# Optimization experiments

Measured on AMD Instinct MI355X. Metric: run time of the kernel, lower is better.

## Reference

```python
import jax, jax.numpy as jnp
import numpy as np

N0, N1, N2 = 100000, 20000, 4000   # nodes per hierarchy level
F, H, C = 128, 128, 10             # num_features, hidden_dim, num_classes
E0, E1, E2 = 1600000, 320000, 64000  # intra-level edges (avg degree 16)
EPS = 1e-5                          # BatchNorm eps


def setup_inputs() -> dict:
    key = jax.random.key(0)
    ks = jax.random.split(key, 16)
    s = 0.05
    return {
        "x": jax.random.normal(ks[0], (N0, F), jnp.float32),
        "ei0": jax.random.randint(ks[1], (2, E0), 0, N0),
        "ei1": jax.random.randint(ks[2], (2, E1), 0, N1),
        "ei2": jax.random.randint(ks[3], (2, E2), 0, N2),
        "parent1": jax.random.randint(ks[4], (N0,), 0, N1),
        "parent2": jax.random.randint(ks[5], (N1,), 0, N2),
        "W0": jax.random.normal(ks[6], (F, H), jnp.float32) * s,
        "b0": jnp.zeros((H,), jnp.float32),
        "W1": jax.random.normal(ks[7], (H, H), jnp.float32) * s,
        "b1": jnp.zeros((H,), jnp.float32),
        "W2": jax.random.normal(ks[8], (H, H), jnp.float32) * s,
        "b2": jnp.zeros((H,), jnp.float32),
        "W3": jax.random.normal(ks[9], (2 * H, H), jnp.float32) * s,
        "b3": jnp.zeros((H,), jnp.float32),
        "W4": jax.random.normal(ks[10], (2 * H, C), jnp.float32) * s,
        "b4": jnp.zeros((C,), jnp.float32),
        "pW": jax.random.normal(ks[11], (4, H, H), jnp.float32) * s,
        "pb": jnp.zeros((4, H), jnp.float32),
        "pgamma": jnp.ones((4, H), jnp.float32),
        "pbeta": jnp.zeros((4, H), jnp.float32),
        "pmean": jax.random.normal(ks[12], (4, H), jnp.float32) * 0.1,
        "pvar": jax.random.uniform(ks[13], (4, H), jnp.float32, 0.5, 1.5),
    }


def _gcn(x, ei, W, b):
    # GCNConv: add self loops, symmetric D^-1/2 (A+I) D^-1/2 normalization.
    n = x.shape[0]
    loops = jnp.arange(n)
    row = jnp.concatenate([ei[0], loops])  # source nodes
    col = jnp.concatenate([ei[1], loops])  # target nodes
    deg = jax.ops.segment_sum(jnp.ones(row.shape, x.dtype), col, num_segments=n)
    dis = deg ** -0.5  # deg >= 1 because of self loops
    norm = dis[row] * dis[col]
    xw = x @ W
    out = jax.ops.segment_sum(norm[:, None] * xw[row], col, num_segments=n)
    return out + b


def _pool_nn(y, W, b, g, beta, mean, var):
    # SEPooling nn: Linear -> ReLU -> BatchNorm1d (eval mode, running stats)
    y = jax.nn.relu(y @ W + b)
    return (y - mean) * (g / jnp.sqrt(var + EPS)) + beta


def reference(x, ei0, ei1, ei2, parent1, parent2,
              W0, b0, W1, b1, W2, b2, W3, b3, W4, b4,
              pW, pb, pgamma, pbeta, pmean, pvar):
    relu = jax.nn.relu
    # down path (dropout is identity in eval mode)
    h0 = relu(_gcn(x, ei0, W0, b0))  # [N0,H]; stored skip xs[0]
    p = jax.ops.segment_sum(h0, parent1, num_segments=N1)  # scatter-add children -> parents
    x1 = relu(_pool_nn(p, pW[0], pb[0], pgamma[0], pbeta[0], pmean[0], pvar[0]))
    h1 = relu(_gcn(x1, ei1, W1, b1))  # [N1,H]; stored skip xs[1]
    p = jax.ops.segment_sum(h1, parent2, num_segments=N2)
    x2 = relu(_pool_nn(p, pW[1], pb[1], pgamma[1], pbeta[1], pmean[1], pvar[1]))
    # up path: conv, unpool (gather parent feature per child), concat skip
    h = relu(_gcn(x2, ei2, W2, b2))  # [N2,H]
    xu = relu(_pool_nn(h[parent2], pW[2], pb[2], pgamma[2], pbeta[2], pmean[2], pvar[2]))  # [N1,H]
    xc = jnp.concatenate([xu, h1], axis=1)  # [N1,2H]
    h = relu(_gcn(xc, ei1, W3, b3))  # [N1,H]
    xu = relu(_pool_nn(h[parent1], pW[3], pb[3], pgamma[3], pbeta[3], pmean[3], pvar[3]))  # [N0,H]
    xc = jnp.concatenate([xu, h0], axis=1)  # [N0,2H]
    out = _gcn(xc, ei0, W4, b4)  # [N0,C]
    return jax.nn.log_softmax(out, axis=-1)
```

## Files before the change

### kernel.cpp

```cpp
#include <hip/hip_runtime.h>
#include <math.h>

#define N0 100000
#define N1 20000
#define N2 4000
#define HDIM 128
#define E0C 1600000
#define E1C 320000
#define E2C 64000
#define EPSBN 1e-5f

typedef unsigned int u32;
typedef float f32x4 __attribute__((ext_vector_type(4)));
typedef short bf16x8 __attribute__((ext_vector_type(8)));

union FragU { uint4 u; bf16x8 h; };
__device__ __forceinline__ bf16x8 asbf(uint4 v) { FragU x; x.u = v; return x.h; }

__device__ __forceinline__ float bl(u32 p) { return __uint_as_float(p << 16); }
__device__ __forceinline__ float bh(u32 p) { return __uint_as_float(p & 0xFFFF0000u); }
__device__ __forceinline__ u32 pack2(float a, float b) {
    u32 ua = __float_as_uint(a), ub = __float_as_uint(b);
    ua = (ua + 0x7FFFu + ((ua >> 16) & 1u)) >> 16;
    ub = (ub + 0x7FFFu + ((ub >> 16) & 1u)) >> 16;
    return ua | (ub << 16);
}

#define OFF0 0
#define OFF1 (N0)
#define OFF2 (N0 + N1)
#define OFF3 (N0 + N1 + N2)
#define OFF4 (N0 + N1 + N2 + N1)
#define OFFT (N0 + N1 + N2 + N1 + N2)

#define S0 (E0C)
#define S1 (E0C + E1C)
#define S2 (E0C + E1C + E2C)
#define S3 (E0C + E1C + E2C + N0)
#define S4 (E0C + E1C + E2C + N0 + N1)

#define NBUCK ((OFFT + 1023) / 1024)
#define ITEMS_PER_BLK 2048
#define NBA ((S4 + ITEMS_PER_BLK - 1) / ITEMS_PER_BLK)
#define BH_N (NBUCK * NBA)
#define NBLK2 ((BH_N + 1023) / 1024)


__device__ __forceinline__ void item_full(int g,
    const int* __restrict__ ei0r, const int* __restrict__ ei0c,
    const int* __restrict__ ei1r, const int* __restrict__ ei1c,
    const int* __restrict__ ei2r, const int* __restrict__ ei2c,
    const int* __restrict__ p1, const int* __restrict__ p2,
    int& concat, int& payload)
{
    if (g < S0)      { concat = ei0c[g];             payload = ei0r[g]; }
    else if (g < S1) { int i = g - S0; concat = OFF1 + ei1c[i]; payload = ei1r[i]; }
    else if (g < S2) { int i = g - S1; concat = OFF2 + ei2c[i]; payload = ei2r[i]; }
    else if (g < S3) { int i = g - S2; concat = OFF3 + p1[i];   payload = i; }
    else             { int i = g - S3; concat = OFF4 + p2[i];   payload = i; }
}

__device__ __forceinline__ int item_concat(int g,
    const int* __restrict__ ei0c, const int* __restrict__ ei1c, const int* __restrict__ ei2c,
    const int* __restrict__ p1, const int* __restrict__ p2)
{
    if (g < S0)      return ei0c[g];
    else if (g < S1) return OFF1 + ei1c[g - S0];
    else if (g < S2) return OFF2 + ei2c[g - S1];
    else if (g < S3) return OFF3 + p1[g - S2];
    else             return OFF4 + p2[g - S3];
}

__global__ __launch_bounds__(256) void binhist_kernel(
    const int* __restrict__ ei0c, const int* __restrict__ ei1c, const int* __restrict__ ei2c,
    const int* __restrict__ p1, const int* __restrict__ p2,
    int* __restrict__ blockHist)
{
    __shared__ int hist[NBUCK];
    int tid = threadIdx.x, blk = blockIdx.x;
    for (int i = tid; i < NBUCK; i += 256) hist[i] = 0;
    __syncthreads();
    int base = blk * ITEMS_PER_BLK;
    #pragma unroll
    for (int k = 0; k < ITEMS_PER_BLK / 256; k++) {
        int g = base + k * 256 + tid;
        if (g < S4) {
            int c = item_concat(g, ei0c, ei1c, ei2c, p1, p2);
            atomicAdd(&hist[c >> 10], 1);
        }
    }
    __syncthreads();
    for (int b = tid; b < NBUCK; b += 256) blockHist[b * NBA + blk] = hist[b];
}

__global__ __launch_bounds__(256) void scan_k1(const int* __restrict__ c, int* __restrict__ bsum, int n) {
    int t = threadIdx.x;
    int base = blockIdx.x * 1024 + t * 4;
    int s = 0;
    #pragma unroll
    for (int j = 0; j < 4; j++) {
        int idx = base + j;
        if (idx < n) s += c[idx];
    }
    #pragma unroll
    for (int o = 32; o > 0; o >>= 1) s += __shfl_down(s, o, 64);
    __shared__ int ws[4];
    if ((t & 63) == 0) ws[t >> 6] = s;
    __syncthreads();
    if (t == 0) bsum[blockIdx.x] = ws[0] + ws[1] + ws[2] + ws[3];
}

__global__ __launch_bounds__(256) void scan_k2(int* __restrict__ bsum, int* __restrict__ totalOut, int nb) {
    int t = threadIdx.x;
    int v = (t < nb) ? bsum[t] : 0;
    __shared__ int ts[256];
    ts[t] = v;
    __syncthreads();
    for (int o = 1; o < 256; o <<= 1) {
        int u = (t >= o) ? ts[t - o] : 0;
        __syncthreads();
        ts[t] += u;
        __syncthreads();
    }
    if (t < nb) bsum[t] = ts[t] - v;
    if (t == nb - 1) *totalOut = ts[t];
}

__global__ __launch_bounds__(256) void scan_k3(const int* __restrict__ c, const int* __restrict__ bsum,
                                               const int* __restrict__ total,
                                               int* __restrict__ S, int n) {
    int t = threadIdx.x;
    int base = blockIdx.x * 1024 + t * 4;
    int v[4];
    #pragma unroll
    for (int j = 0; j < 4; j++) v[j] = (base + j < n) ? c[base + j] : 0;
    int tsum = v[0] + v[1] + v[2] + v[3];
    __shared__ int ts[256];
    ts[t] = tsum;
    __syncthreads();
    for (int o = 1; o < 256; o <<= 1) {
        int u = (t >= o) ? ts[t - o] : 0;
        __syncthreads();
        ts[t] += u;
        __syncthreads();
    }
    int run = bsum[blockIdx.x] + ts[t] - tsum;
    #pragma unroll
    for (int j = 0; j < 4; j++) {
        if (base + j < n) { S[base + j] = run; run += v[j]; }
    }
    if (blockIdx.x == 0 && t == 0) S[n] = *total;
}

__global__ __launch_bounds__(256) void binfill_kernel(
    const int* __restrict__ ei0r, const int* __restrict__ ei0c,
    const int* __restrict__ ei1r, const int* __restrict__ ei1c,
    const int* __restrict__ ei2r, const int* __restrict__ ei2c,
    const int* __restrict__ p1, const int* __restrict__ p2,
    const int* __restrict__ OfsAbs, u32* __restrict__ binPair)
{
    __shared__ int cur[NBUCK];
    int tid = threadIdx.x, blk = blockIdx.x;
    for (int i = tid; i < NBUCK; i += 256) cur[i] = OfsAbs[i * NBA + blk];
    __syncthreads();
    int base = blk * ITEMS_PER_BLK;
    #pragma unroll
    for (int k = 0; k < ITEMS_PER_BLK / 256; k++) {
        int g = base + k * 256 + tid;
        if (g < S4) {
            int c, p;
            item_full(g, ei0r, ei0c, ei1r, ei1c, ei2r, ei2c, p1, p2, c, p);
            int pos = atomicAdd(&cur[c >> 10], 1);
            binPair[pos] = ((u32)(c & 1023) << 17) | (u32)p;
        }
    }
}

__global__ __launch_bounds__(1024) void bucket_build_kernel(
    const u32* __restrict__ binPair, const int* __restrict__ OfsAbs,
    int* __restrict__ rpAll, int* __restrict__ srcU,
    float* __restrict__ dis0, float* __restrict__ dis1, float* __restrict__ dis2)
{
    __shared__ int cnt_l[1024];
    __shared__ int rp_l[1024];
    __shared__ int ts2[1024];
    int b = blockIdx.x, tid = threadIdx.x;
    int start = OfsAbs[b * NBA];
    int end = (b + 1 < NBUCK) ? OfsAbs[(b + 1) * NBA] : S4;
    int d0 = b << 10;
    int nd = OFFT - d0; if (nd > 1024) nd = 1024;

    cnt_l[tid] = 0;
    __syncthreads();
    for (int i = start + tid; i < end; i += 1024) {
        u32 e = binPair[i];
        atomicAdd(&cnt_l[e >> 17], 1);
    }
    __syncthreads();
    int v = cnt_l[tid];
    ts2[tid] = v;
    __syncthreads();
    for (int o = 1; o < 1024; o <<= 1) {
        int u = (tid >= o) ? ts2[tid - o] : 0;
        __syncthreads();
        ts2[tid] += u;
        __syncthreads();
    }
    rp_l[tid] = ts2[tid] - v;
    __syncthreads();
    if (tid < nd) {
        int g = d0 + tid;
        rpAll[g] = start + rp_l[tid];
        float dv = rsqrtf((float)(v + 1));
        if (g < OFF1) dis0[g] = dv;
        else if (g < OFF2) dis1[g - OFF1] = dv;
        else if (g < OFF3) dis2[g - OFF2] = dv;
    }
    if (b == NBUCK - 1 && tid == 0) rpAll[OFFT] = S4;
    __syncthreads();
    for (int i = start + tid; i < end; i += 1024) {
        u32 e = binPair[i];
        int pos = start + atomicAdd(&rp_l[e >> 17], 1);
        srcU[pos] = (int)(e & 0x1FFFFu);
    }
}

__global__ void bn_pre_kernel(const float* __restrict__ g, const float* __restrict__ beta,
                              const float* __restrict__ mean, const float* __restrict__ var,
                              float* __restrict__ scale, float* __restrict__ shift) {
    int i = blockIdx.x * blockDim.x + threadIdx.x;
    if (i < 4 * HDIM) {
        float s = g[i] * rsqrtf(var[i] + EPSBN);
        scale[i] = s;
        shift[i] = beta[i] - mean[i] * s;
    }
}


#define G128_LOAD(sym, off) u32 sym = y[(long long)srcl[e + off] * 64 + lane]

__global__ __launch_bounds__(256) void gather128_kernel(
    const int* __restrict__ rp, const int* __restrict__ srcl,
    const u32* __restrict__ y, const float* __restrict__ dis,
    const float* __restrict__ bias, u32* __restrict__ h, int n)
{
    int wid = (int)((blockIdx.x * 256 + threadIdx.x) >> 6);
    int lane = threadIdx.x & 63;
    if (wid >= n) return;
    u32 self = y[(long long)wid * 64 + lane];
    float ax = bl(self), ay = bh(self);
    int e = rp[wid], e1 = rp[wid + 1];
    for (; e + 7 < e1; e += 8) {
        G128_LOAD(p0, 0); G128_LOAD(p1, 1); G128_LOAD(p2, 2); G128_LOAD(p3, 3);
        G128_LOAD(p4, 4); G128_LOAD(p5, 5); G128_LOAD(p6, 6); G128_LOAD(p7, 7);
        ax += ((bl(p0) + bl(p1)) + (bl(p2) + bl(p3))) + ((bl(p4) + bl(p5)) + (bl(p6) + bl(p7)));
        ay += ((bh(p0) + bh(p1)) + (bh(p2) + bh(p3))) + ((bh(p4) + bh(p5)) + (bh(p6) + bh(p7)));
    }
    if (e + 3 < e1) {
        G128_LOAD(p0, 0); G128_LOAD(p1, 1); G128_LOAD(p2, 2); G128_LOAD(p3, 3);
        ax += (bl(p0) + bl(p1)) + (bl(p2) + bl(p3));
        ay += (bh(p0) + bh(p1)) + (bh(p2) + bh(p3));
        e += 4;
    }
    if (e + 1 < e1) {
        G128_LOAD(p0, 0); G128_LOAD(p1, 1);
        ax += bl(p0) + bl(p1);
        ay += bh(p0) + bh(p1);
        e += 2;
    }
    if (e < e1) {
        G128_LOAD(p0, 0);
        ax += bl(p0); ay += bh(p0);
    }
    float d = dis[wid];
    float2 b = ((const float2*)bias)[lane];
    float r0 = fmaxf(fmaf(d, ax, b.x), 0.f);
    float r1 = fmaxf(fmaf(d, ay, b.y), 0.f);
    h[(long long)wid * 64 + lane] = pack2(r0, r1);
}

__global__ __launch_bounds__(256) void gather10_lsm_kernel(
    const int* __restrict__ rp, const int* __restrict__ srcl,
    const u32* __restrict__ y4, const float* __restrict__ dis,
    const float* __restrict__ bias, float* __restrict__ out, int n)
{
    int c = blockIdx.x * blockDim.x + threadIdx.x;
    if (c >= n) return;
    float acc[10];
    {
        long long base = (long long)c * 8;
        uint4 q = *(const uint4*)(y4 + base);
        u32 q4 = y4[base + 4];
        acc[0] = bl(q.x); acc[1] = bh(q.x);
        acc[2] = bl(q.y); acc[3] = bh(q.y);
        acc[4] = bl(q.z); acc[5] = bh(q.z);
        acc[6] = bl(q.w); acc[7] = bh(q.w);
        acc[8] = bl(q4);  acc[9] = bh(q4);
    }
    int e = rp[c], e1 = rp[c + 1];
    for (; e + 3 < e1; e += 4) {
        long long bA = (long long)srcl[e] * 8;
        long long bB = (long long)srcl[e + 1] * 8;
        long long bC = (long long)srcl[e + 2] * 8;
        long long bD = (long long)srcl[e + 3] * 8;
        uint4 qa = *(const uint4*)(y4 + bA); u32 qa4 = y4[bA + 4];
        uint4 qb = *(const uint4*)(y4 + bB); u32 qb4 = y4[bB + 4];
        uint4 qc = *(const uint4*)(y4 + bC); u32 qc4 = y4[bC + 4];
        uint4 qd = *(const uint4*)(y4 + bD); u32 qd4 = y4[bD + 4];
        acc[0] += (bl(qa.x) + bl(qb.x)) + (bl(qc.x) + bl(qd.x));
        acc[1] += (bh(qa.x) + bh(qb.x)) + (bh(qc.x) + bh(qd.x));
        acc[2] += (bl(qa.y) + bl(qb.y)) + (bl(qc.y) + bl(qd.y));
        acc[3] += (bh(qa.y) + bh(qb.y)) + (bh(qc.y) + bh(qd.y));
        acc[4] += (bl(qa.z) + bl(qb.z)) + (bl(qc.z) + bl(qd.z));
        acc[5] += (bh(qa.z) + bh(qb.z)) + (bh(qc.z) + bh(qd.z));
        acc[6] += (bl(qa.w) + bl(qb.w)) + (bl(qc.w) + bl(qd.w));
        acc[7] += (bh(qa.w) + bh(qb.w)) + (bh(qc.w) + bh(qd.w));
        acc[8] += (bl(qa4) + bl(qb4)) + (bl(qc4) + bl(qd4));
        acc[9] += (bh(qa4) + bh(qb4)) + (bh(qc4) + bh(qd4));
    }
    for (; e < e1; e++) {
        long long bA = (long long)srcl[e] * 8;
        uint4 qa = *(const uint4*)(y4 + bA);
        u32 qa4 = y4[bA + 4];
        acc[0] += bl(qa.x); acc[1] += bh(qa.x);
        acc[2] += bl(qa.y); acc[3] += bh(qa.y);
        acc[4] += bl(qa.z); acc[5] += bh(qa.z);
        acc[6] += bl(qa.w); acc[7] += bh(qa.w);
        acc[8] += bl(qa4);  acc[9] += bh(qa4);
    }
    float d = dis[c];
    float m = -1e30f;
    #pragma unroll
    for (int k = 0; k < 10; k++) {
        acc[k] = fmaf(d, acc[k], bias[k]);
        m = fmaxf(m, acc[k]);
    }
    float s = 0.f;
    #pragma unroll
    for (int k = 0; k < 10; k++) s += expf(acc[k] - m);
    float ls = logf(s);
    #pragma unroll
    for (int k = 0; k < 10; k++) out[(long long)c * 10 + k] = acc[k] - m - ls;
}

__global__ __launch_bounds__(256) void mm128_kernel(
    const void* __restrict__ Av, const float* __restrict__ W,
    u32* __restrict__ out, int M,
    const float* __restrict__ dis,
    const u32* __restrict__ gsrc, const int* __restrict__ gidx,
    const float* __restrict__ bias,
    const float* __restrict__ bnscale, const float* __restrict__ bnshift,
    int pool, int afp32,
    const int* __restrict__ pp, const int* __restrict__ childl, int apool)
{
    __shared__ u32 WL[8192];
    int tid = threadIdx.x;

    #pragma unroll
    for (int it = 0; it < 32; it++) {
        int flat = it * 256 + tid;
        int i = flat & 3;
        int ln = (flat >> 2) & 63;
        int s = (flat >> 8) & 3;
        int t = flat >> 10;
        int mm = ln & 15, qq = ln >> 4;
        int k0 = s * 32 + qq * 8 + 2 * i;
        int col = t * 16 + mm;
        WL[flat] = pack2(W[k0 * 128 + col], W[(k0 + 1) * 128 + col]);
    }
    __syncthreads();

    int lane = tid & 63;
    int w = tid >> 6;
    int m = lane & 15, q = lane >> 4;
    int row = blockIdx.x * 64 + w * 16 + m;
    bool live = (row < M);

    uint4 xb[4];
    if (live) {
        if (apool) {
            float fa[32];
            #pragma unroll
            for (int i = 0; i < 32; i++) fa[i] = 0.f;
            const u32* Hb = (const u32*)Av;
            int e = pp[row], eE = pp[row + 1];
            for (; e < eE; e++) {
                long long cb = (long long)childl[e] * 64;
                #pragma unroll
                for (int s = 0; s < 4; s++) {
                    uint4 vv = *(const uint4*)(Hb + cb + s * 16 + q * 4);
                    fa[s * 8 + 0] += bl(vv.x); fa[s * 8 + 1] += bh(vv.x);
                    fa[s * 8 + 2] += bl(vv.y); fa[s * 8 + 3] += bh(vv.y);
                    fa[s * 8 + 4] += bl(vv.z); fa[s * 8 + 5] += bh(vv.z);
                    fa[s * 8 + 6] += bl(vv.w); fa[s * 8 + 7] += bh(vv.w);
                }
            }
            #pragma unroll
            for (int s = 0; s < 4; s++) {
                xb[s].x = pack2(fa[s * 8 + 0], fa[s * 8 + 1]);
                xb[s].y = pack2(fa[s * 8 + 2], fa[s * 8 + 3]);
                xb[s].z = pack2(fa[s * 8 + 4], fa[s * 8 + 5]);
                xb[s].w = pack2(fa[s * 8 + 6], fa[s * 8 + 7]);
            }
        } else if (afp32) {
            const float* Af = (const float*)Av;
            #pragma unroll
            for (int s = 0; s < 4; s++) {
                const float4* p = (const float4*)(Af + (long long)row * 128 + s * 32 + q * 8);
                float4 f0 = p[0], f1 = p[1];
                xb[s].x = pack2(f0.x, f0.y);
                xb[s].y = pack2(f0.z, f0.w);
                xb[s].z = pack2(f1.x, f1.y);
                xb[s].w = pack2(f1.z, f1.w);
            }
        } else {
            const u32* Ab = (const u32*)Av;
            #pragma unroll
            for (int s = 0; s < 4; s++)
                xb[s] = *(const uint4*)(Ab + (long long)row * 64 + s * 16 + q * 4);
        }
    } else {
        xb[0] = xb[1] = xb[2] = xb[3] = make_uint4(0u, 0u, 0u, 0u);
    }

    float d = 1.0f;
    if (dis && live) d = dis[row];
    long long gbase = (gsrc && live) ? (long long)gidx[row] * 64 : 0;

    #pragma unroll
    for (int t = 0; t < 8; t++) {
        f32x4 acc = {0.f, 0.f, 0.f, 0.f};
        #pragma unroll
        for (int s = 0; s < 4; s++) {
            uint4 wa = *(const uint4*)&WL[((t * 4 + s) * 64 + lane) * 4];
            acc = __builtin_amdgcn_mfma_f32_16x16x32_bf16(asbf(wa), asbf(xb[s]), acc, 0, 0, 0);
        }
        if (live) {
            float v0 = acc[0], v1 = acc[1], v2 = acc[2], v3 = acc[3];
            int cbase = t * 16 + q * 4;
            if (gsrc) {
                uint2 g = *(const uint2*)(gsrc + gbase + (cbase >> 1));
                v0 += bl(g.x); v1 += bh(g.x);
                v2 += bl(g.y); v3 += bh(g.y);
            }
            if (pool) {
                float4 bb = *(const float4*)(bias + cbase);
                float4 sc = *(const float4*)(bnscale + cbase);
                float4 sh = *(const float4*)(bnshift + cbase);
                v0 = fmaxf(fmaxf(v0 + bb.x, 0.f) * sc.x + sh.x, 0.f);
                v1 = fmaxf(fmaxf(v1 + bb.y, 0.f) * sc.y + sh.y, 0.f);
                v2 = fmaxf(fmaxf(v2 + bb.z, 0.f) * sc.z + sh.z, 0.f);
                v3 = fmaxf(fmaxf(v3 + bb.w, 0.f) * sc.w + sh.w, 0.f);
            }
            v0 *= d; v1 *= d; v2 *= d; v3 *= d;
            uint2 st;
            st.x = pack2(v0, v1);
            st.y = pack2(v2, v3);
            *(uint2*)(out + (long long)row * 64 + (cbase >> 1)) = st;
        }
    }
}

__global__ __launch_bounds__(256) void mm10_kernel(
    const u32* __restrict__ A, const float* __restrict__ W,
    float* __restrict__ out, int M)
{
    __shared__ float Ws[128 * 10];
    for (int i = threadIdx.x; i < 1280; i += 256) Ws[i] = W[i];
    __syncthreads();
    int row = blockIdx.x * blockDim.x + threadIdx.x;
    if (row >= M) return;
    const uint4* a = (const uint4*)(A + (long long)row * 64);
    float acc[10] = {0, 0, 0, 0, 0, 0, 0, 0, 0, 0};
    #pragma unroll 4
    for (int i = 0; i < 16; i++) {
        uint4 av = a[i];
        int k = i * 8;
        float f[8] = { bl(av.x), bh(av.x), bl(av.y), bh(av.y),
                       bl(av.z), bh(av.z), bl(av.w), bh(av.w) };
        #pragma unroll
        for (int j = 0; j < 8; j++) {
            #pragma unroll
            for (int cc = 0; cc < 10; cc++)
                acc[cc] += f[j] * Ws[(k + j) * 10 + cc];
        }
    }
    #pragma unroll
    for (int cc = 0; cc < 10; cc++) out[(long long)row * 10 + cc] = acc[cc];
}

__global__ __launch_bounds__(256) void mm10p_kernel(
    const u32* __restrict__ A, const float* __restrict__ W,
    u32* __restrict__ outp, int M,
    const float* __restrict__ dis,
    const float* __restrict__ gsrc, const int* __restrict__ gidx)
{
    __shared__ float Ws[128 * 10];
    for (int i = threadIdx.x; i < 1280; i += 256) Ws[i] = W[i];
    __syncthreads();
    int row = blockIdx.x * blockDim.x + threadIdx.x;
    if (row >= M) return;
    const uint4* a = (const uint4*)(A + (long long)row * 64);
    float acc[10] = {0, 0, 0, 0, 0, 0, 0, 0, 0, 0};
    #pragma unroll 4
    for (int i = 0; i < 16; i++) {
        uint4 av = a[i];
        int k = i * 8;
        float f[8] = { bl(av.x), bh(av.x), bl(av.y), bh(av.y),
                       bl(av.z), bh(av.z), bl(av.w), bh(av.w) };
        #pragma unroll
        for (int j = 0; j < 8; j++) {
            #pragma unroll
            for (int cc = 0; cc < 10; cc++)
                acc[cc] += f[j] * Ws[(k + j) * 10 + cc];
        }
    }
    float d = dis[row];
    const float* g = gsrc + (long long)gidx[row] * 10;
    long long base = (long long)row * 8;
    #pragma unroll
    for (int j = 0; j < 5; j++) {
        float v0 = (acc[2 * j] + g[2 * j]) * d;
        float v1 = (acc[2 * j + 1] + g[2 * j + 1]) * d;
        outp[base + j] = pack2(v0, v1);
    }
}


extern "C" void kernel_launch(void* const* d_in, const int* in_sizes, int n_in,
                              void* d_out, int out_size, void* d_ws, size_t ws_size,
                              hipStream_t stream) {
    const float* x       = (const float*)d_in[0];
    const int*   ei0     = (const int*)d_in[1];
    const int*   ei1     = (const int*)d_in[2];
    const int*   ei2     = (const int*)d_in[3];
    const int*   parent1 = (const int*)d_in[4];
    const int*   parent2 = (const int*)d_in[5];
    const float* W0 = (const float*)d_in[6];
    const float* b0 = (const float*)d_in[7];
    const float* W1 = (const float*)d_in[8];
    const float* b1 = (const float*)d_in[9];
    const float* W2 = (const float*)d_in[10];
    const float* b2 = (const float*)d_in[11];
    const float* W3 = (const float*)d_in[12];
    const float* b3 = (const float*)d_in[13];
    const float* W4 = (const float*)d_in[14];
    const float* b4 = (const float*)d_in[15];
    const float* pW = (const float*)d_in[16];
    const float* pb = (const float*)d_in[17];
    const float* pg = (const float*)d_in[18];
    const float* pbeta = (const float*)d_in[19];
    const float* pmean = (const float*)d_in[20];
    const float* pvar  = (const float*)d_in[21];
    float* out = (float*)d_out;

    char* ws = (char*)d_ws;
    size_t off = 0;
    auto alloc = [&](size_t nbytes) -> char* {
        char* p = ws + off;
        off += ((nbytes + 255) / 256) * 256;
        return p;
    };
    float* dis0 = (float*)alloc(N0 * 4);
    float* dis1 = (float*)alloc(N1 * 4);
    float* dis2 = (float*)alloc(N2 * 4);
    float* bnscale = (float*)alloc(4 * HDIM * 4);
    float* bnshift = (float*)alloc(4 * HDIM * 4);
    float* W1b = (float*)alloc((size_t)N1 * 10 * 4);
    u32* Y   = (u32*)alloc((size_t)N0 * 64 * 4);
    u32* H0  = (u32*)alloc((size_t)N0 * 64 * 4);
    u32* H1  = (u32*)alloc((size_t)N1 * 64 * 4);
    u32* X1  = (u32*)alloc((size_t)N1 * 64 * 4);
    u32* HU1 = (u32*)alloc((size_t)N1 * 64 * 4);
    u32* U1  = (u32*)alloc((size_t)N1 * 64 * 4);
    u32* X2  = (u32*)alloc((size_t)N2 * 64 * 4);
    u32* H2  = (u32*)alloc((size_t)N2 * 64 * 4);
    u32* U2  = (u32*)alloc((size_t)N2 * 64 * 4);
    u32* V2  = (u32*)alloc((size_t)N2 * 64 * 4);
    u32* Y4p = (u32*)alloc((size_t)N0 * 8 * 4);
    int* rpAll = (int*)alloc((size_t)(OFFT + 1) * 4);
    int* srcU  = (int*)alloc((size_t)S4 * 4);
    int* blockHist = (int*)alloc((size_t)BH_N * 4);
    int* OfsAbs    = (int*)alloc((size_t)(BH_N + 1) * 4);
    u32* binPair   = (u32*)alloc((size_t)S4 * 4);
    int* bsum   = (int*)alloc(NBLK2 * 4);
    int* totalb = (int*)alloc(4);

    const int B = 256;
    auto G = [](long long t) { return (unsigned)((t + 255) / 256); };
    auto G64 = [](long long m) { return (unsigned)((m + 63) / 64); };

    binhist_kernel<<<NBA, B, 0, stream>>>(
        ei0 + E0C, ei1 + E1C, ei2 + E2C, parent1, parent2, blockHist);
    scan_k1<<<NBLK2, B, 0, stream>>>(blockHist, bsum, BH_N);
    scan_k2<<<1, B, 0, stream>>>(bsum, totalb, NBLK2);
    scan_k3<<<NBLK2, B, 0, stream>>>(blockHist, bsum, totalb, OfsAbs, BH_N);
    binfill_kernel<<<NBA, B, 0, stream>>>(
        ei0, ei0 + E0C, ei1, ei1 + E1C, ei2, ei2 + E2C, parent1, parent2, OfsAbs, binPair);
    bucket_build_kernel<<<NBUCK, 1024, 0, stream>>>(
        binPair, OfsAbs, rpAll, srcU, dis0, dis1, dis2);
    bn_pre_kernel<<<2, B, 0, stream>>>(pg, pbeta, pmean, pvar, bnscale, bnshift);

    mm128_kernel<<<G64(N0), B, 0, stream>>>(
        x, W0, Y, N0, dis0, nullptr, nullptr, nullptr, nullptr, nullptr, 0, 1,
        nullptr, nullptr, 0);
    gather128_kernel<<<G((long long)N0 * 64), B, 0, stream>>>(rpAll + OFF0, srcU, Y, dis0, b0, H0, N0);

    mm128_kernel<<<G64(N1), B, 0, stream>>>(
        H0, pW, X1, N1, nullptr, nullptr, nullptr, pb, bnscale, bnshift, 1, 0,
        rpAll + OFF3, srcU, 1);

    mm128_kernel<<<G64(N1), B, 0, stream>>>(
        X1, W1, Y, N1, dis1, nullptr, nullptr, nullptr, nullptr, nullptr, 0, 0,
        nullptr, nullptr, 0);
    gather128_kernel<<<G((long long)N1 * 64), B, 0, stream>>>(rpAll + OFF1, srcU, Y, dis1, b1, H1, N1);

    mm128_kernel<<<G64(N2), B, 0, stream>>>(
        H1, pW + 128 * 128, X2, N2, nullptr, nullptr, nullptr, pb + 128, bnscale + 128, bnshift + 128, 1, 0,
        rpAll + OFF4, srcU, 1);

    mm128_kernel<<<G64(N2), B, 0, stream>>>(
        X2, W2, Y, N2, dis2, nullptr, nullptr, nullptr, nullptr, nullptr, 0, 0,
        nullptr, nullptr, 0);
    gather128_kernel<<<G((long long)N2 * 64), B, 0, stream>>>(rpAll + OFF2, srcU, Y, dis2, b2, H2, N2);

    mm128_kernel<<<G64(N2), B, 0, stream>>>(
        H2, pW + 2 * 128 * 128, U2, N2, nullptr, nullptr, nullptr, pb + 256, bnscale + 256, bnshift + 256, 1, 0,
        nullptr, nullptr, 0);
    mm128_kernel<<<G64(N2), B, 0, stream>>>(
        U2, W3, V2, N2, nullptr, nullptr, nullptr, nullptr, nullptr, nullptr, 0, 0,
        nullptr, nullptr, 0);

    mm128_kernel<<<G64(N1), B, 0, stream>>>(
        H1, W3 + 128 * 128, Y, N1, dis1, V2, parent2, nullptr, nullptr, nullptr, 0, 0,
        nullptr, nullptr, 0);
    gather128_kernel<<<G((long long)N1 * 64), B, 0, stream>>>(rpAll + OFF1, srcU, Y, dis1, b3, HU1, N1);

    mm128_kernel<<<G64(N1), B, 0, stream>>>(
        HU1, pW + 3 * 128 * 128, U1, N1, nullptr, nullptr, nullptr, pb + 384, bnscale + 384, bnshift + 384, 1, 0,
        nullptr, nullptr, 0);
    mm10_kernel<<<G(N1), B, 0, stream>>>(U1, W4, W1b, N1);

    mm10p_kernel<<<G(N0), B, 0, stream>>>(H0, W4 + 128 * 10, Y4p, N0, dis0, W1b, parent1);
    gather10_lsm_kernel<<<G(N0), B, 0, stream>>>(rpAll + OFF0, srcU, Y4p, dis0, b4, out, N0);
}
```

Before: 432.4 us.

## Pre-pack weights once and fuse back-to-back pool-MLP and GCN matmuls

The bf16 MFMA-layout packing of all nine 128x128 weight matrices moves into extra blocks of the histogram kernel, so each mm128 block just copies a prepacked tile into LDS instead of repacking from fp32. Consecutive pairs of matmuls (pool Linear+ReLU+BN followed by the GCN weight multiply) are fused into a new mm128x2 kernel that keeps the intermediate tile in LDS. This removes the intermediate X1/X2/U2 round-trips and several launches. The BN precompute is also folded into scan_k2. The cost is extra LDS per block for the fused kernel, which may lower occupancy.

```diff
diff --git a/kernel.cpp b/kernel.cpp
--- a/kernel.cpp
+++ b/kernel.cpp
@@ -45,6 +45,8 @@
 #define BH_N (NBUCK * NBA)
 #define NBLK2 ((BH_N + 1023) / 1024)
 
+#define NWMAT 9
+
 
 __device__ __forceinline__ void item_full(int g,
     const int* __restrict__ ei0r, const int* __restrict__ ei0c,
@@ -74,10 +76,37 @@
 __global__ __launch_bounds__(256) void binhist_kernel(
     const int* __restrict__ ei0c, const int* __restrict__ ei1c, const int* __restrict__ ei2c,
     const int* __restrict__ p1, const int* __restrict__ p2,
-    int* __restrict__ blockHist)
+    int* __restrict__ blockHist,
+    const float* __restrict__ W0p, const float* __restrict__ W1p,
+    const float* __restrict__ W2p, const float* __restrict__ W3p,
+    const float* __restrict__ pWp, u32* __restrict__ Wpk)
 {
     __shared__ int hist[NBUCK];
     int tid = threadIdx.x, blk = blockIdx.x;
+    if (blk >= NBA) {
+        int b = blk - NBA;
+        const float* src;
+        if (b == 0) src = W0p;
+        else if (b == 1) src = W1p;
+        else if (b == 2) src = W2p;
+        else if (b == 3) src = W3p;
+        else if (b == 4) src = W3p + 128 * 128;
+        else src = pWp + (b - 5) * 128 * 128;
+        u32* dst = Wpk + b * 8192;
+        #pragma unroll
+        for (int it = 0; it < 32; it++) {
+            int flat = it * 256 + tid;
+            int i = flat & 3;
+            int ln = (flat >> 2) & 63;
+            int s = (flat >> 8) & 3;
+            int t = flat >> 10;
+            int mm = ln & 15, qq = ln >> 4;
+            int k0 = s * 32 + qq * 8 + 2 * i;
+            int col = t * 16 + mm;
+            dst[flat] = pack2(src[k0 * 128 + col], src[(k0 + 1) * 128 + col]);
+        }
+        return;
+    }
     for (int i = tid; i < NBUCK; i += 256) hist[i] = 0;
     __syncthreads();
     int base = blk * ITEMS_PER_BLK;
@@ -110,8 +139,19 @@
     if (t == 0) bsum[blockIdx.x] = ws[0] + ws[1] + ws[2] + ws[3];
 }
 
-__global__ __launch_bounds__(256) void scan_k2(int* __restrict__ bsum, int* __restrict__ totalOut, int nb) {
+__global__ __launch_bounds__(256) void scan_k2(int* __restrict__ bsum, int* __restrict__ totalOut, int nb,
+    const float* __restrict__ g, const float* __restrict__ beta,
+    const float* __restrict__ mean, const float* __restrict__ var,
+    float* __restrict__ scale, float* __restrict__ shift)
+{
     int t = threadIdx.x;
+    #pragma unroll
+    for (int j = 0; j < 2; j++) {
+        int i = j * 256 + t;
+        float s = g[i] * rsqrtf(var[i] + EPSBN);
+        scale[i] = s;
+        shift[i] = beta[i] - mean[i] * s;
+    }
     int v = (t < nb) ? bsum[t] : 0;
     __shared__ int ts[256];
     ts[t] = v;
@@ -222,17 +262,6 @@
         u32 e = binPair[i];
         int pos = start + atomicAdd(&rp_l[e >> 17], 1);
         srcU[pos] = (int)(e & 0x1FFFFu);
-    }
-}
-
-__global__ void bn_pre_kernel(const float* __restrict__ g, const float* __restrict__ beta,
-                              const float* __restrict__ mean, const float* __restrict__ var,
-                              float* __restrict__ scale, float* __restrict__ shift) {
-    int i = blockIdx.x * blockDim.x + threadIdx.x;
-    if (i < 4 * HDIM) {
-        float s = g[i] * rsqrtf(var[i] + EPSBN);
-        scale[i] = s;
-        shift[i] = beta[i] - mean[i] * s;
     }
 }
 
@@ -344,7 +373,7 @@
 }
 
 __global__ __launch_bounds__(256) void mm128_kernel(
-    const void* __restrict__ Av, const float* __restrict__ W,
+    const void* __restrict__ Av, const u32* __restrict__ Wp,
     u32* __restrict__ out, int M,
     const float* __restrict__ dis,
     const u32* __restrict__ gsrc, const int* __restrict__ gidx,
@@ -355,18 +384,11 @@
 {
     __shared__ u32 WL[8192];
     int tid = threadIdx.x;
-
-    #pragma unroll
-    for (int it = 0; it < 32; it++) {
-        int flat = it * 256 + tid;
-        int i = flat & 3;
-        int ln = (flat >> 2) & 63;
-        int s = (flat >> 8) & 3;
-        int t = flat >> 10;
-        int mm = ln & 15, qq = ln >> 4;
-        int k0 = s * 32 + qq * 8 + 2 * i;
-        int col = t * 16 + mm;
-        WL[flat] = pack2(W[k0 * 128 + col], W[(k0 + 1) * 128 + col]);
+    {
+        const uint4* ws4 = (const uint4*)Wp;
+        uint4* wd4 = (uint4*)WL;
+        #pragma unroll
+        for (int it = 0; it < 8; it++) wd4[it * 256 + tid] = ws4[it * 256 + tid];
     }
     __syncthreads();
 
@@ -453,6 +475,123 @@
                 v3 = fmaxf(fmaxf(v3 + bb.w, 0.f) * sc.w + sh.w, 0.f);
             }
             v0 *= d; v1 *= d; v2 *= d; v3 *= d;
+            uint2 st;
+            st.x = pack2(v0, v1);
+            st.y = pack2(v2, v3);
+            *(uint2*)(out + (long long)row * 64 + (cbase >> 1)) = st;
+        }
+    }
+}
+
+#define TLP 68
+__global__ __launch_bounds__(256) void mm128x2_kernel(
+    const u32* __restrict__ Av, const u32* __restrict__ Wa, const u32* __restrict__ Wb,
+    u32* __restrict__ out, int M,
+    const float* __restrict__ dis2,
+    const float* __restrict__ bias1,
+    const float* __restrict__ bnscale1, const float* __restrict__ bnshift1,
+    const int* __restrict__ pp, const int* __restrict__ childl, int apool)
+{
+    __shared__ u32 WL[8192];
+    __shared__ u32 TL[64 * TLP];
+    int tid = threadIdx.x;
+    {
+        const uint4* ws4 = (const uint4*)Wa;
+        uint4* wd4 = (uint4*)WL;
+        #pragma unroll
+        for (int it = 0; it < 8; it++) wd4[it * 256 + tid] = ws4[it * 256 + tid];
+    }
+    __syncthreads();
+
+    int lane = tid & 63;
+    int w = tid >> 6;
+    int m = lane & 15, q = lane >> 4;
+    int row = blockIdx.x * 64 + w * 16 + m;
+    bool live = (row < M);
+
+    uint4 xb[4];
+    if (live) {
+        if (apool) {
+            float fa[32];
+            #pragma unroll
+            for (int i = 0; i < 32; i++) fa[i] = 0.f;
+            int e = pp[row], eE = pp[row + 1];
+            for (; e < eE; e++) {
+                long long cb = (long long)childl[e] * 64;
+                #pragma unroll
+                for (int s = 0; s < 4; s++) {
+                    uint4 vv = *(const uint4*)(Av + cb + s * 16 + q * 4);
+                    fa[s * 8 + 0] += bl(vv.x); fa[s * 8 + 1] += bh(vv.x);
+                    fa[s * 8 + 2] += bl(vv.y); fa[s * 8 + 3] += bh(vv.y);
+                    fa[s * 8 + 4] += bl(vv.z); fa[s * 8 + 5] += bh(vv.z);
+                    fa[s * 8 + 6] += bl(vv.w); fa[s * 8 + 7] += bh(vv.w);
+                }
+            }
+            #pragma unroll
+            for (int s = 0; s < 4; s++) {
+                xb[s].x = pack2(fa[s * 8 + 0], fa[s * 8 + 1]);
+                xb[s].y = pack2(fa[s * 8 + 2], fa[s * 8 + 3]);
+                xb[s].z = pack2(fa[s * 8 + 4], fa[s * 8 + 5]);
+                xb[s].w = pack2(fa[s * 8 + 6], fa[s * 8 + 7]);
+            }
+        } else {
+            #pragma unroll
+            for (int s = 0; s < 4; s++)
+                xb[s] = *(const uint4*)(Av + (long long)row * 64 + s * 16 + q * 4);
+        }
+    } else {
+        xb[0] = xb[1] = xb[2] = xb[3] = make_uint4(0u, 0u, 0u, 0u);
+    }
+
+    u32* tl = TL + (w * 16 + m) * TLP;
+
+    #pragma unroll
+    for (int t = 0; t < 8; t++) {
+        f32x4 acc = {0.f, 0.f, 0.f, 0.f};
+        #pragma unroll
+        for (int s = 0; s < 4; s++) {
+            uint4 wa4 = *(const uint4*)&WL[((t * 4 + s) * 64 + lane) * 4];
+            acc = __builtin_amdgcn_mfma_f32_16x16x32_bf16(asbf(wa4), asbf(xb[s]), acc, 0, 0, 0);
+        }
+        int cbase = t * 16 + q * 4;
+        float4 bb = *(const float4*)(bias1 + cbase);
+        float4 sc = *(const float4*)(bnscale1 + cbase);
+        float4 sh = *(const float4*)(bnshift1 + cbase);
+        float v0 = fmaxf(fmaxf(acc[0] + bb.x, 0.f) * sc.x + sh.x, 0.f);
+        float v1 = fmaxf(fmaxf(acc[1] + bb.y, 0.f) * sc.y + sh.y, 0.f);
+        float v2 = fmaxf(fmaxf(acc[2] + bb.z, 0.f) * sc.z + sh.z, 0.f);
+        float v3 = fmaxf(fmaxf(acc[3] + bb.w, 0.f) * sc.w + sh.w, 0.f);
+        uint2 st;
+        st.x = pack2(v0, v1);
+        st.y = pack2(v2, v3);
+        *(uint2*)&tl[t * 8 + q * 2] = st;
+    }
+    __syncthreads();
+    {
+        const uint4* ws4 = (const uint4*)Wb;
+        uint4* wd4 = (uint4*)WL;
+        #pragma unroll
+        for (int it = 0; it < 8; it++) wd4[it * 256 + tid] = ws4[it * 256 + tid];
+    }
+    __syncthreads();
+
+    #pragma unroll
+    for (int s = 0; s < 4; s++)
+        xb[s] = *(const uint4*)&tl[s * 16 + q * 4];
+    float d = 1.0f;
+    if (dis2 && live) d = dis2[row];
+
+    #pragma unroll
+    for (int t = 0; t < 8; t++) {
+        f32x4 acc = {0.f, 0.f, 0.f, 0.f};
+        #pragma unroll
+        for (int s = 0; s < 4; s++) {
+            uint4 wa4 = *(const uint4*)&WL[((t * 4 + s) * 64 + lane) * 4];
+            acc = __builtin_amdgcn_mfma_f32_16x16x32_bf16(asbf(wa4), asbf(xb[s]), acc, 0, 0, 0);
+        }
+        if (live) {
+            int cbase = t * 16 + q * 4;
+            float v0 = acc[0] * d, v1 = acc[1] * d, v2 = acc[2] * d, v3 = acc[3] * d;
             uint2 st;
             st.x = pack2(v0, v1);
             st.y = pack2(v2, v3);
@@ -570,14 +709,12 @@
     u32* Y   = (u32*)alloc((size_t)N0 * 64 * 4);
     u32* H0  = (u32*)alloc((size_t)N0 * 64 * 4);
     u32* H1  = (u32*)alloc((size_t)N1 * 64 * 4);
-    u32* X1  = (u32*)alloc((size_t)N1 * 64 * 4);
     u32* HU1 = (u32*)alloc((size_t)N1 * 64 * 4);
     u32* U1  = (u32*)alloc((size_t)N1 * 64 * 4);
-    u32* X2  = (u32*)alloc((size_t)N2 * 64 * 4);
     u32* H2  = (u32*)alloc((size_t)N2 * 64 * 4);
-    u32* U2  = (u32*)alloc((size_t)N2 * 64 * 4);
     u32* V2  = (u32*)alloc((size_t)N2 * 64 * 4);
     u32* Y4p = (u32*)alloc((size_t)N0 * 8 * 4);
+    u32* Wpk = (u32*)alloc((size_t)NWMAT * 8192 * 4);
     int* rpAll = (int*)alloc((size_t)(OFFT + 1) * 4);
     int* srcU  = (int*)alloc((size_t)S4 * 4);
     int* blockHist = (int*)alloc((size_t)BH_N * 4);
@@ -590,54 +727,43 @@
     auto G = [](long long t) { return (unsigned)((t + 255) / 256); };
     auto G64 = [](long long m) { return (unsigned)((m + 63) / 64); };
 
-    binhist_kernel<<<NBA, B, 0, stream>>>(
-        ei0 + E0C, ei1 + E1C, ei2 + E2C, parent1, parent2, blockHist);
+    binhist_kernel<<<NBA + NWMAT, B, 0, stream>>>(
+        ei0 + E0C, ei1 + E1C, ei2 + E2C, parent1, parent2, blockHist,
+        W0, W1, W2, W3, pW, Wpk);
     scan_k1<<<NBLK2, B, 0, stream>>>(blockHist, bsum, BH_N);
-    scan_k2<<<1, B, 0, stream>>>(bsum, totalb, NBLK2);
+    scan_k2<<<1, B, 0, stream>>>(bsum, totalb, NBLK2, pg, pbeta, pmean, pvar, bnscale, bnshift);
     scan_k3<<<NBLK2, B, 0, stream>>>(blockHist, bsum, totalb, OfsAbs, BH_N);
     binfill_kernel<<<NBA, B, 0, stream>>>(
         ei0, ei0 + E0C, ei1, ei1 + E1C, ei2, ei2 + E2C, parent1, parent2, OfsAbs, binPair);
     bucket_build_kernel<<<NBUCK, 1024, 0, stream>>>(
         binPair, OfsAbs, rpAll, srcU, dis0, dis1, dis2);
-    bn_pre_kernel<<<2, B, 0, stream>>>(pg, pbeta, pmean, pvar, bnscale, bnshift);
 
     mm128_kernel<<<G64(N0), B, 0, stream>>>(
-        x, W0, Y, N0, dis0, nullptr, nullptr, nullptr, nullptr, nullptr, 0, 1,
+        x, Wpk + 0 * 8192, Y, N0, dis0, nullptr, nullptr, nullptr, nullptr, nullptr, 0, 1,
         nullptr, nullptr, 0);
     gather128_kernel<<<G((long long)N0 * 64), B, 0, stream>>>(rpAll + OFF0, srcU, Y, dis0, b0, H0, N0);
 
+    mm128x2_kernel<<<G64(N1), B, 0, stream>>>(
+        H0, Wpk + 5 * 8192, Wpk + 1 * 8192, Y, N1, dis1,
+        pb, bnscale, bnshift, rpAll + OFF3, srcU, 1);
+    gather128_kernel<<<G((long long)N1 * 64), B, 0, stream>>>(rpAll + OFF1, srcU, Y, dis1, b1, H1, N1);
+
+    mm128x2_kernel<<<G64(N2), B, 0, stream>>>(
+        H1, Wpk + 6 * 8192, Wpk + 2 * 8192, Y, N2, dis2,
+        pb + 128, bnscale + 128, bnshift + 128, rpAll + OFF4, srcU, 1);
+    gather128_kernel<<<G((long long)N2 * 64), B, 0, stream>>>(rpAll + OFF2, srcU, Y, dis2, b2, H2, N2);
+
+    mm128x2_kernel<<<G64(N2), B, 0, stream>>>(
+        H2, Wpk + 7 * 8192, Wpk + 3 * 8192, V2, N2, nullptr,
+        pb + 256, bnscale + 256, bnshift + 256, nullptr, nullptr, 0);
+
     mm128_kernel<<<G64(N1), B, 0, stream>>>(
-        H0, pW, X1, N1, nullptr, nullptr, nullptr, pb, bnscale, bnshift, 1, 0,
-        rpAll + OFF3, srcU, 1);
-
-    mm128_kernel<<<G64(N1), B, 0, stream>>>(
-        X1, W1, Y, N1, dis1, nullptr, nullptr, nullptr, nullptr, nullptr, 0, 0,
-        nullptr, nullptr, 0);
-    gather128_kernel<<<G((long long)N1 * 64), B, 0, stream>>>(rpAll + OFF1, srcU, Y, dis1, b1, H1, N1);
-
-    mm128_kernel<<<G64(N2), B, 0, stream>>>(
-        H1, pW + 128 * 128, X2, N2, nullptr, nullptr, nullptr, pb + 128, bnscale + 128, bnshift + 128, 1, 0,
-        rpAll + OFF4, srcU, 1);
-
-    mm128_kernel<<<G64(N2), B, 0, stream>>>(
-        X2, W2, Y, N2, dis2, nullptr, nullptr, nullptr, nullptr, nullptr, 0, 0,
-        nullptr, nullptr, 0);
-    gather128_kernel<<<G((long long)N2 * 64), B, 0, stream>>>(rpAll + OFF2, srcU, Y, dis2, b2, H2, N2);
-
-    mm128_kernel<<<G64(N2), B, 0, stream>>>(
-        H2, pW + 2 * 128 * 128, U2, N2, nullptr, nullptr, nullptr, pb + 256, bnscale + 256, bnshift + 256, 1, 0,
-        nullptr, nullptr, 0);
-    mm128_kernel<<<G64(N2), B, 0, stream>>>(
-        U2, W3, V2, N2, nullptr, nullptr, nullptr, nullptr, nullptr, nullptr, 0, 0,
-        nullptr, nullptr, 0);
-
-    mm128_kernel<<<G64(N1), B, 0, stream>>>(
-        H1, W3 + 128 * 128, Y, N1, dis1, V2, parent2, nullptr, nullptr, nullptr, 0, 0,
+        H1, Wpk + 4 * 8192, Y, N1, dis1, V2, parent2, nullptr, nullptr, nullptr, 0, 0,
         nullptr, nullptr, 0);
     gather128_kernel<<<G((long long)N1 * 64), B, 0, stream>>>(rpAll + OFF1, srcU, Y, dis1, b3, HU1, N1);
 
     mm128_kernel<<<G64(N1), B, 0, stream>>>(
-        HU1, pW + 3 * 128 * 128, U1, N1, nullptr, nullptr, nullptr, pb + 384, bnscale + 384, bnshift + 384, 1, 0,
+        HU1, Wpk + 8 * 8192, U1, N1, nullptr, nullptr, nullptr, pb + 384, bnscale + 384, bnshift + 384, 1, 0,
         nullptr, nullptr, 0);
     mm10_kernel<<<G(N1), B, 0, stream>>>(U1, W4, W1b, N1);
 
```

After: 392.4 us. -9.2%, faster.
